# Kernel tuning notes

Measured on AMD Instinct MI355X. Metric: run time of the kernel, lower is better.

## Reference

```python
import jax, jax.numpy as jnp
import numpy as np

B, V_IN, V_OUT, F_IN, F_OUT, N_CP = 100000, 128, 128, 512, 512, 16
DIM_H = max(V_IN, V_OUT)  # hidden_vectors=None -> max(dim_vectors_in, dim_vectors_out)
EPS = 1e-8


def setup_inputs() -> dict:
    key = jax.random.key(0)
    ks = jax.random.split(key, 9)
    u = lambda k, shape, scale: jax.random.uniform(k, shape, jnp.float32, -scale, scale)
    wh_k = 1.0 / np.sqrt(V_IN).astype(np.float32)
    wu_k = 1.0 / np.sqrt(DIM_H + N_CP).astype(np.float32)
    f_in = DIM_H + N_CP + F_IN  # 656
    kf = 1.0 / np.sqrt(f_in).astype(np.float32)
    kg = 1.0 / np.sqrt(F_OUT).astype(np.float32)
    return {
        "feats": jax.random.normal(ks[0], (B, F_IN), jnp.float32),
        "vectors": jax.random.normal(ks[1], (B, V_IN, 3), jnp.float32),
        "Wh": u(ks[2], (V_IN, DIM_H), wh_k),
        "Wcp": u(ks[3], (V_IN, 2 * N_CP), wh_k),
        "Wu": u(ks[4], (DIM_H + N_CP, V_OUT), wu_k),
        "Wf": u(ks[5], (f_in, F_OUT), kf),      # torch Linear weight, stored (in,out)
        "bf": u(ks[6], (F_OUT,), kf),
        "Wg": u(ks[7], (F_OUT, V_OUT), kg),
        "bg": u(ks[8], (V_OUT,), kg),
    }


def reference(feats, vectors, Wh, Wcp, Wu, Wf, bf, Wg, bg):
    # vectors: [b, v_in, 3]; mix vector channels (matmul acts per xyz component c)
    Vh = jnp.einsum('bvc,vh->bhc', vectors, Wh)            # [b, dim_h, 3]
    # cross-product features
    Vcp = jnp.einsum('bvc,vp->bpc', vectors, Wcp)          # [b, 2*n_cp, 3]
    cp = jnp.cross(Vcp[:, :N_CP], Vcp[:, N_CP:])           # [b, n_cp, 3]
    Vh = jnp.concatenate([Vh, cp], axis=1)                 # [b, dim_h+n_cp, 3]
    Vu = jnp.einsum('bkc,ko->boc', Vh, Wu)                 # [b, v_out, 3]
    # clamped L2 norm over xyz
    sh = jnp.sqrt(jnp.maximum(jnp.sum(Vh * Vh, axis=-1), EPS))  # [b, dim_h+n_cp]
    s = jnp.concatenate([feats, sh], axis=1)               # [b, dim_h+n_cp+f_in]
    feats_out = jax.nn.silu(s @ Wf + bf)                   # [b, f_out]
    gating = feats_out @ Wg + bg                           # [b, v_out]
    vectors_out = jax.nn.sigmoid(gating)[..., None] * Vu   # [b, v_out, 3]
    return feats_out, vectors_out
```

## Files before the change

### kernel.cpp

```cpp
#include <hip/hip_runtime.h>

#define BATCH 100000
#define M3 300000
#define VECBASE 51200000
#define KP 704

typedef float fl4  __attribute__((ext_vector_type(4)));
typedef float f32x4 __attribute__((ext_vector_type(4)));
typedef short s16x4 __attribute__((ext_vector_type(4)));
typedef short s16x8 __attribute__((ext_vector_type(8)));

__device__ __forceinline__ short f2bf(float f) {
  unsigned int u = __float_as_uint(f);
  u += 0x7fffu + ((u >> 16) & 1u);
  return (short)(u >> 16);
}
__device__ __forceinline__ float bf2f(short s) {
  return __uint_as_float(((unsigned int)(unsigned short)s) << 16);
}
__device__ __forceinline__ s16x8 pack8(fl4 a, fl4 b) {
  s16x8 o;
  o[0] = f2bf(a[0]); o[1] = f2bf(a[1]); o[2] = f2bf(a[2]); o[3] = f2bf(a[3]);
  o[4] = f2bf(b[0]); o[5] = f2bf(b[1]); o[6] = f2bf(b[2]); o[7] = f2bf(b[3]);
  return o;
}
__device__ __forceinline__ void glds16(const void* g, void* l) {
  __builtin_amdgcn_global_load_lds((const __attribute__((address_space(1))) void*)g,
                                   (__attribute__((address_space(3))) void*)l, 16, 0, 0);
}

__global__ __launch_bounds__(256) void prep_w(
    const float* __restrict__ feats, const float* __restrict__ Wh,
    const float* __restrict__ Wcp, const float* __restrict__ Wu,
    const float* __restrict__ Wf, const float* __restrict__ Wg,
    short* __restrict__ Ab, short* __restrict__ WB1, short* __restrict__ WuTp,
    short* __restrict__ WfT, short* __restrict__ WgT) {
  const int tid = blockIdx.x * 256 + threadIdx.x;
  const int stride = gridDim.x * 256;
  for (int i = tid; i < 6400000; i += stride) {
    int b = i >> 6, kk = (i & 63) * 8;
    fl4 v0 = *reinterpret_cast<const fl4*>(&feats[(size_t)b * 512 + kk]);
    fl4 v1 = *reinterpret_cast<const fl4*>(&feats[(size_t)b * 512 + kk + 4]);
    *(s16x8*)&Ab[(size_t)b * KP + kk] = pack8(v0, v1);
  }
  for (int gid = tid; gid < 466944; gid += stride) {
    if (gid < 20480) {
      int n = gid >> 7, k = gid & 127;
      WB1[gid] = f2bf(n < 128 ? Wh[k * 128 + n] : Wcp[k * 32 + (n - 128)]);
    } else if (gid < 40960) {
      int i = gid - 20480;
      int o = i / 160, k = i - o * 160;
      WuTp[i] = k < 144 ? f2bf(Wu[k * 128 + o]) : (short)0;
    } else if (gid < 401408) {
      int i = gid - 40960;
      int n = i / KP, k = i - n * KP;
      WfT[i] = k < 656 ? f2bf(Wf[k * 512 + n]) : (short)0;
    } else {
      int i = gid - 401408;
      int n = i >> 9, k = i & 511;
      WgT[i] = f2bf(Wg[k * 128 + n]);
    }
  }
}

__global__ __launch_bounds__(256) void geo_fused(
    const float* __restrict__ vecs, const short* __restrict__ WB1,
    const short* __restrict__ WuTp, short* __restrict__ Ab,
    short* __restrict__ Vub) {
  __shared__ __align__(16) short U[192 * 168];
  const int t = threadIdx.x;
  const int b0 = blockIdx.x * 64;
  const int row0 = blockIdx.x * 192;

#pragma unroll
  for (int it = 0; it < 8; ++it) {
    int fi = (it * 256 + t) * 12;
    int bl = fi / 384;
    int rem = fi - bl * 384;
    int v0 = rem / 3;
    int b = b0 + bl;
    fl4 x = (fl4){0.f, 0.f, 0.f, 0.f}, y = x, z = x;
    if (b < BATCH) {
      const float* p = &vecs[(size_t)b * 384 + rem];
      x = *(const fl4*)p; y = *(const fl4*)(p + 4); z = *(const fl4*)(p + 8);
    }
    float vc[3][4] = {{x[0], x[3], y[2], z[1]},
                      {x[1], y[0], y[3], z[2]},
                      {x[2], y[1], z[0], z[3]}};
#pragma unroll
    for (int c = 0; c < 3; ++c) {
      int row = bl * 3 + c;
      s16x4 q;
#pragma unroll
      for (int e = 0; e < 4; ++e) q[e] = f2bf(vc[c][e]);
      int off = (row << 8) + (v0 << 1);
      *(s16x4*)((char*)U + (off ^ ((row & 7) << 4))) = q;
    }
  }
  __syncthreads();

  const int lane = t & 63, wv = t >> 6;
  const int wr = wv >> 1, wc = wv & 1;
  const int lr = lane & 15, lk = lane >> 4;

  {
    f32x4 acc[6][5];
#pragma unroll
    for (int i = 0; i < 6; ++i)
#pragma unroll
      for (int j = 0; j < 5; ++j) acc[i][j] = (f32x4){0.f, 0.f, 0.f, 0.f};
#pragma unroll
    for (int kk = 0; kk < 4; ++kk) {
      s16x8 af[6], bq[5];
#pragma unroll
      for (int mi = 0; mi < 6; ++mi) {
        int row = wr * 96 + mi * 16 + lr;
        int off = (row << 8) + (kk << 6) + (lk << 4);
        af[mi] = *(const s16x8*)((const char*)U + (off ^ ((row & 7) << 4)));
      }
#pragma unroll
      for (int ni = 0; ni < 5; ++ni)
        bq[ni] = *reinterpret_cast<const s16x8*>(
            &WB1[(wc * 80 + ni * 16 + lr) * 128 + (kk << 5) + (lk << 3)]);
      __builtin_amdgcn_s_setprio(1);
#pragma unroll
      for (int mi = 0; mi < 6; ++mi)
#pragma unroll
        for (int ni = 0; ni < 5; ++ni)
          acc[mi][ni] = __builtin_amdgcn_mfma_f32_16x16x32_bf16(af[mi], bq[ni], acc[mi][ni], 0, 0, 0);
      __builtin_amdgcn_s_setprio(0);
    }
    __syncthreads();
#pragma unroll
    for (int mi = 0; mi < 6; ++mi)
#pragma unroll
      for (int ni = 0; ni < 5; ++ni) {
        int col = wc * 80 + ni * 16 + lr;
#pragma unroll
        for (int r = 0; r < 4; ++r) {
          int row = wr * 96 + mi * 16 + lk * 4 + r;
          U[row * 168 + col] = f2bf(acc[mi][ni][r]);
        }
      }
  }
  __syncthreads();

  {
    int bl = t >> 2, pj = t & 3;
    int gb = b0 + bl;
    float shcp[4];
#pragma unroll
    for (int q = 0; q < 4; ++q) {
      int p = pj * 4 + q;
      float ax = bf2f(U[(bl * 3 + 0) * 168 + 128 + p]);
      float ay = bf2f(U[(bl * 3 + 1) * 168 + 128 + p]);
      float az = bf2f(U[(bl * 3 + 2) * 168 + 128 + p]);
      float bx = bf2f(U[(bl * 3 + 0) * 168 + 144 + p]);
      float by = bf2f(U[(bl * 3 + 1) * 168 + 144 + p]);
      float bz = bf2f(U[(bl * 3 + 2) * 168 + 144 + p]);
      float cx = ay * bz - az * by;
      float cy = az * bx - ax * bz;
      float cz = ax * by - ay * bx;
      U[(bl * 3 + 0) * 168 + 128 + p] = f2bf(cx);
      U[(bl * 3 + 1) * 168 + 128 + p] = f2bf(cy);
      U[(bl * 3 + 2) * 168 + 128 + p] = f2bf(cz);
      U[(bl * 3 + 0) * 168 + 144 + p] = 0;
      U[(bl * 3 + 1) * 168 + 144 + p] = 0;
      U[(bl * 3 + 2) * 168 + 144 + p] = 0;
      shcp[q] = sqrtf(fmaxf(cx * cx + cy * cy + cz * cz, 1e-8f));
    }
    if (gb < BATCH) {
#pragma unroll
      for (int q = 0; q < 4; ++q)
        Ab[(size_t)gb * KP + 512 + 128 + pj * 4 + q] = f2bf(shcp[q]);
#pragma unroll
      for (int z = 0; z < 12; ++z)
        Ab[(size_t)gb * KP + 512 + 144 + pj * 12 + z] = 0;
    }
  }
  {
    int bl = t >> 2, kq = t & 3;
    int gb = b0 + bl;
    if (gb < BATCH) {
#pragma unroll
      for (int j = 0; j < 4; ++j) {
        int k = kq * 32 + j * 8;
        s16x8 r0 = *(const s16x8*)&U[(bl * 3 + 0) * 168 + k];
        s16x8 r1 = *(const s16x8*)&U[(bl * 3 + 1) * 168 + k];
        s16x8 r2 = *(const s16x8*)&U[(bl * 3 + 2) * 168 + k];
        s16x8 o;
#pragma unroll
        for (int e = 0; e < 8; ++e) {
          float x = bf2f(r0[e]), y = bf2f(r1[e]), z = bf2f(r2[e]);
          o[e] = f2bf(sqrtf(fmaxf(x * x + y * y + z * z, 1e-8f)));
        }
        *(s16x8*)&Ab[(size_t)gb * KP + 512 + k] = o;
      }
    }
  }
  __syncthreads();

  {
    f32x4 acc2[6][4];
#pragma unroll
    for (int i = 0; i < 6; ++i)
#pragma unroll
      for (int j = 0; j < 4; ++j) acc2[i][j] = (f32x4){0.f, 0.f, 0.f, 0.f};
#pragma unroll
    for (int kk = 0; kk < 5; ++kk) {
      s16x8 af[6], bq[4];
#pragma unroll
      for (int mi = 0; mi < 6; ++mi) {
        int row = wr * 96 + mi * 16 + lr;
        af[mi] = *(const s16x8*)&U[row * 168 + (kk << 5) + (lk << 3)];
      }
#pragma unroll
      for (int ni = 0; ni < 4; ++ni)
        bq[ni] = *reinterpret_cast<const s16x8*>(
            &WuTp[(wc * 64 + ni * 16 + lr) * 160 + (kk << 5) + (lk << 3)]);
      __builtin_amdgcn_s_setprio(1);
#pragma unroll
      for (int mi = 0; mi < 6; ++mi)
#pragma unroll
        for (int ni = 0; ni < 4; ++ni)
          acc2[mi][ni] = __builtin_amdgcn_mfma_f32_16x16x32_bf16(af[mi], bq[ni], acc2[mi][ni], 0, 0, 0);
      __builtin_amdgcn_s_setprio(0);
    }
#pragma unroll
    for (int mi = 0; mi < 6; ++mi)
#pragma unroll
      for (int ni = 0; ni < 4; ++ni) {
        int col = wc * 64 + ni * 16 + lr;
#pragma unroll
        for (int r = 0; r < 4; ++r) {
          int row = row0 + wr * 96 + mi * 16 + lk * 4 + r;
          if (row < M3) Vub[(size_t)row * 128 + col] = f2bf(acc2[mi][ni][r]);
        }
      }
  }
}

__global__ __launch_bounds__(512, 4) void gemm_feats(
    const short* __restrict__ Ab, const short* __restrict__ WfT,
    const float* __restrict__ bfv, float* __restrict__ out,
    short* __restrict__ fob) {
  const int bid = blockIdx.x;
  const int xcd = bid & 7, bi = bid >> 3;
  const int swz = (xcd < 4 ? xcd * 196 : 784 + (xcd - 4) * 195) + bi;
  const int mt = swz >> 1, nt = swz & 1;
  const int row0 = mt << 7, n0 = nt << 8;
  const int t = threadIdx.x;
  const int lane = t & 63, wv = t >> 6;
  const int wr = wv >> 2, wc = wv & 3;
  const int lr = lane & 15, lk = lane >> 4;

  __shared__ __align__(16) short S[(128 + 256) * 64];
  short* As = S;
  short* Bs = S + 128 * 64;

  const short* srcA[2]; int adof[2];
#pragma unroll
  for (int j = 0; j < 2; ++j) {
    int cid = j * 512 + t;
    int row = cid >> 3, ch = cid & 7;
    srcA[j] = &Ab[(size_t)min(row0 + row, BATCH - 1) * KP + (ch ^ (row & 7)) * 8];
    adof[j] = cid * 8;
  }
  const short* srcB[4]; int bdof[4];
#pragma unroll
  for (int j = 0; j < 4; ++j) {
    int cid = j * 512 + t;
    int row = cid >> 3, ch = cid & 7;
    srcB[j] = &WfT[(size_t)(n0 + row) * KP + (ch ^ (row & 7)) * 8];
    bdof[j] = cid * 8;
  }

  f32x4 acc[4][4];
#pragma unroll
  for (int i = 0; i < 4; ++i)
#pragma unroll
    for (int j = 0; j < 4; ++j) acc[i][j] = (f32x4){0.f, 0.f, 0.f, 0.f};

  for (int ks = 0; ks < 11; ++ks) {
    const int k0 = ks << 6;
    __syncthreads();
    glds16(srcA[0] + k0, &As[adof[0]]);
    glds16(srcA[1] + k0, &As[adof[1]]);
#pragma unroll
    for (int j = 0; j < 4; ++j) glds16(srcB[j] + k0, &Bs[bdof[j]]);
    __syncthreads();
#pragma unroll
    for (int kk = 0; kk < 2; ++kk) {
      s16x8 af[4], bq[4];
#pragma unroll
      for (int mi = 0; mi < 4; ++mi) {
        int rw = wr * 64 + mi * 16 + lr;
        af[mi] = *(const s16x8*)&As[rw * 64 + (((kk << 2) + lk) ^ (rw & 7)) * 8];
      }
#pragma unroll
      for (int ni = 0; ni < 4; ++ni) {
        int rn = wc * 64 + ni * 16 + lr;
        bq[ni] = *(const s16x8*)&Bs[rn * 64 + (((kk << 2) + lk) ^ (rn & 7)) * 8];
      }
      __builtin_amdgcn_s_setprio(1);
#pragma unroll
      for (int mi = 0; mi < 4; ++mi)
#pragma unroll
        for (int ni = 0; ni < 4; ++ni)
          acc[mi][ni] = __builtin_amdgcn_mfma_f32_16x16x32_bf16(af[mi], bq[ni], acc[mi][ni], 0, 0, 0);
      __builtin_amdgcn_s_setprio(0);
    }
  }

  float* Ls = (float*)S;
#pragma unroll
  for (int g = 0; g < 8; ++g) {
    __syncthreads();
    if (wr == (g >> 2)) {
      int mi = g & 3;
#pragma unroll
      for (int ni = 0; ni < 4; ++ni) {
        int colL = wc * 64 + ni * 16 + lr;
        float bb = bfv[n0 + colL];
#pragma unroll
        for (int rr = 0; rr < 4; ++rr) {
          float x = acc[mi][ni][rr] + bb;
          Ls[(lk * 4 + rr) * 256 + colL] = x / (1.f + __expf(-x));
        }
      }
    }
    __syncthreads();
    {
      int rowL = t >> 5, seg = t & 31;
      int grow = row0 + g * 16 + rowL;
      if (grow < BATCH) {
        const float* p = &Ls[rowL * 256 + seg * 8];
        fl4 a = *(const fl4*)p, b = *(const fl4*)(p + 4);
        float* po = &out[(size_t)grow * 512 + n0 + seg * 8];
        *(fl4*)po = a; *(fl4*)(po + 4) = b;
        *(s16x8*)&fob[(size_t)grow * 512 + n0 + seg * 8] = pack8(a, b);
      }
    }
  }
}

__global__ __launch_bounds__(512, 4) void gemm_gate(
    const short* __restrict__ fob, const short* __restrict__ WgT,
    const float* __restrict__ bg, const short* __restrict__ Vub,
    float* __restrict__ out) {
  const int bid = blockIdx.x;
  const int xcd = bid & 7, bi = bid >> 3;
  const int swz = (xcd < 7 ? xcd * 49 : 343 + (xcd - 7) * 48) + bi;
  const int row0 = swz << 8;
  const int t = threadIdx.x;
  const int lane = t & 63, wv = t >> 6;
  const int wr = wv >> 1, wc = wv & 1;
  const int lr = lane & 15, lk = lane >> 4;

  __shared__ __align__(16) short S[(256 + 128) * 64];
  short* As = S;
  short* Bs = S + 256 * 64;

  const short* srcA[4]; int adof[4];
#pragma unroll
  for (int j = 0; j < 4; ++j) {
    int cid = j * 512 + t;
    int row = cid >> 3, ch = cid & 7;
    srcA[j] = &fob[(size_t)min(row0 + row, BATCH - 1) * 512 + (ch ^ (row & 7)) * 8];
    adof[j] = cid * 8;
  }
  const short* srcB[2]; int bdof[2];
#pragma unroll
  for (int j = 0; j < 2; ++j) {
    int cid = j * 512 + t;
    int row = cid >> 3, ch = cid & 7;
    srcB[j] = &WgT[(size_t)row * 512 + (ch ^ (row & 7)) * 8];
    bdof[j] = cid * 8;
  }

  f32x4 acc[4][4];
#pragma unroll
  for (int i = 0; i < 4; ++i)
#pragma unroll
    for (int j = 0; j < 4; ++j) acc[i][j] = (f32x4){0.f, 0.f, 0.f, 0.f};

  for (int ks = 0; ks < 8; ++ks) {
    const int k0 = ks << 6;
    __syncthreads();
#pragma unroll
    for (int j = 0; j < 4; ++j) glds16(srcA[j] + k0, &As[adof[j]]);
    glds16(srcB[0] + k0, &Bs[bdof[0]]);
    glds16(srcB[1] + k0, &Bs[bdof[1]]);
    __syncthreads();
#pragma unroll
    for (int kk = 0; kk < 2; ++kk) {
      s16x8 af[4], bq[4];
#pragma unroll
      for (int mi = 0; mi < 4; ++mi) {
        int rw = wr * 64 + mi * 16 + lr;
        af[mi] = *(const s16x8*)&As[rw * 64 + (((kk << 2) + lk) ^ (rw & 7)) * 8];
      }
#pragma unroll
      for (int ni = 0; ni < 4; ++ni) {
        int rn = wc * 64 + ni * 16 + lr;
        bq[ni] = *(const s16x8*)&Bs[rn * 64 + (((kk << 2) + lk) ^ (rn & 7)) * 8];
      }
      __builtin_amdgcn_s_setprio(1);
#pragma unroll
      for (int mi = 0; mi < 4; ++mi)
#pragma unroll
        for (int ni = 0; ni < 4; ++ni)
          acc[mi][ni] = __builtin_amdgcn_mfma_f32_16x16x32_bf16(af[mi], bq[ni], acc[mi][ni], 0, 0, 0);
      __builtin_amdgcn_s_setprio(0);
    }
  }

#pragma unroll
  for (int ni = 0; ni < 4; ++ni) {
    int col = wc * 64 + ni * 16 + lr;
    float bb = bg[col];
#pragma unroll
    for (int mi = 0; mi < 4; ++mi) {
      int rbase = row0 + wr * 64 + mi * 16 + lk * 4;
#pragma unroll
      for (int rr = 0; rr < 4; ++rr) {
        int gr = rbase + rr;
        if (gr < BATCH) {
          float x = acc[mi][ni][rr] + bb;
          float gate = 1.f / (1.f + __expf(-x));
          size_t vb = (size_t)(3 * gr) * 128 + col;
          float* po = &out[VECBASE + ((size_t)gr * 128 + col) * 3];
          po[0] = gate * bf2f(Vub[vb]);
          po[1] = gate * bf2f(Vub[vb + 128]);
          po[2] = gate * bf2f(Vub[vb + 256]);
        }
      }
    }
  }
}

extern "C" void kernel_launch(void* const* d_in, const int* in_sizes, int n_in,
                              void* d_out, int out_size, void* d_ws, size_t ws_size,
                              hipStream_t stream) {
  const float* feats = (const float*)d_in[0];
  const float* vecs  = (const float*)d_in[1];
  const float* Wh    = (const float*)d_in[2];
  const float* Wcp   = (const float*)d_in[3];
  const float* Wu    = (const float*)d_in[4];
  const float* Wf    = (const float*)d_in[5];
  const float* bfv   = (const float*)d_in[6];
  const float* Wg    = (const float*)d_in[7];
  const float* bg    = (const float*)d_in[8];
  float* out = (float*)d_out;

  char* ws = (char*)d_ws;
  short* Ab   = (short*)ws;
  short* Vub  = (short*)(ws + 140800000);
  short* fob  = (short*)(ws + 217600000);
  short* WfT  = (short*)(ws + 320000000);
  short* WgT  = (short*)(ws + 320720896);
  short* WB1  = (short*)(ws + 320851968);
  short* WuTp = (short*)(ws + 320892928);

  hipLaunchKernelGGL(prep_w,     dim3(2048), dim3(256), 0, stream,
                     feats, Wh, Wcp, Wu, Wf, Wg, Ab, WB1, WuTp, WfT, WgT);
  hipLaunchKernelGGL(geo_fused,  dim3(1563), dim3(256), 0, stream,
                     vecs, WB1, WuTp, Ab, Vub);
  hipLaunchKernelGGL(gemm_feats, dim3(1564), dim3(512), 0, stream,
                     Ab, WfT, bfv, out, fob);
  hipLaunchKernelGGL(gemm_gate,  dim3(391),  dim3(512), 0, stream,
                     fob, WgT, bg, Vub, out);
}
```

Before: 432.9 us.

## Double-buffer feature GEMM K-loop and halve geo kernel batch tile

The feature GEMM now uses two LDS buffers with 32-wide K slices, issuing async global-to-LDS loads two stages ahead and synchronising with raw s_waitcnt/s_barrier, so load latency overlaps MFMA work instead of a sync-load-sync per step. The geo kernel processes 32 batch rows per block instead of 64, doubling the grid and shrinking LDS and accumulator usage to raise occupancy. Bounds checks are dropped because 100000 divides evenly by 32. The hand-written vmcnt counts must match the number of outstanding loads, and the K-slice swizzle changed to fit the narrower tiles.

```diff
diff --git a/kernel.cpp b/kernel.cpp
--- a/kernel.cpp
+++ b/kernel.cpp
@@ -28,6 +28,8 @@
   __builtin_amdgcn_global_load_lds((const __attribute__((address_space(1))) void*)g,
                                    (__attribute__((address_space(3))) void*)l, 16, 0, 0);
 }
+#define WAITBAR(N) asm volatile("s_waitcnt vmcnt(" #N ")\ns_barrier" ::: "memory")
+#define RAWBAR()   asm volatile("s_barrier" ::: "memory")
 
 __global__ __launch_bounds__(256) void prep_w(
     const float* __restrict__ feats, const float* __restrict__ Wh,
@@ -67,23 +69,19 @@
     const float* __restrict__ vecs, const short* __restrict__ WB1,
     const short* __restrict__ WuTp, short* __restrict__ Ab,
     short* __restrict__ Vub) {
-  __shared__ __align__(16) short U[192 * 168];
+  __shared__ __align__(16) short U[96 * 168];
   const int t = threadIdx.x;
-  const int b0 = blockIdx.x * 64;
-  const int row0 = blockIdx.x * 192;
-
-#pragma unroll
-  for (int it = 0; it < 8; ++it) {
+  const int b0 = blockIdx.x * 32;
+  const int row0 = blockIdx.x * 96;
+
+#pragma unroll
+  for (int it = 0; it < 4; ++it) {
     int fi = (it * 256 + t) * 12;
     int bl = fi / 384;
     int rem = fi - bl * 384;
     int v0 = rem / 3;
-    int b = b0 + bl;
-    fl4 x = (fl4){0.f, 0.f, 0.f, 0.f}, y = x, z = x;
-    if (b < BATCH) {
-      const float* p = &vecs[(size_t)b * 384 + rem];
-      x = *(const fl4*)p; y = *(const fl4*)(p + 4); z = *(const fl4*)(p + 8);
-    }
+    const float* p = &vecs[(size_t)(b0 + bl) * 384 + rem];
+    fl4 x = *(const fl4*)p, y = *(const fl4*)(p + 4), z = *(const fl4*)(p + 8);
     float vc[3][4] = {{x[0], x[3], y[2], z[1]},
                       {x[1], y[0], y[3], z[2]},
                       {x[2], y[1], z[0], z[3]}};
@@ -104,17 +102,17 @@
   const int lr = lane & 15, lk = lane >> 4;
 
   {
-    f32x4 acc[6][5];
-#pragma unroll
-    for (int i = 0; i < 6; ++i)
+    f32x4 acc[3][5];
+#pragma unroll
+    for (int i = 0; i < 3; ++i)
 #pragma unroll
       for (int j = 0; j < 5; ++j) acc[i][j] = (f32x4){0.f, 0.f, 0.f, 0.f};
 #pragma unroll
     for (int kk = 0; kk < 4; ++kk) {
-      s16x8 af[6], bq[5];
-#pragma unroll
-      for (int mi = 0; mi < 6; ++mi) {
-        int row = wr * 96 + mi * 16 + lr;
+      s16x8 af[3], bq[5];
+#pragma unroll
+      for (int mi = 0; mi < 3; ++mi) {
+        int row = wr * 48 + mi * 16 + lr;
         int off = (row << 8) + (kk << 6) + (lk << 4);
         af[mi] = *(const s16x8*)((const char*)U + (off ^ ((row & 7) << 4)));
       }
@@ -124,7 +122,7 @@
             &WB1[(wc * 80 + ni * 16 + lr) * 128 + (kk << 5) + (lk << 3)]);
       __builtin_amdgcn_s_setprio(1);
 #pragma unroll
-      for (int mi = 0; mi < 6; ++mi)
+      for (int mi = 0; mi < 3; ++mi)
 #pragma unroll
         for (int ni = 0; ni < 5; ++ni)
           acc[mi][ni] = __builtin_amdgcn_mfma_f32_16x16x32_bf16(af[mi], bq[ni], acc[mi][ni], 0, 0, 0);
@@ -132,13 +130,13 @@
     }
     __syncthreads();
 #pragma unroll
-    for (int mi = 0; mi < 6; ++mi)
+    for (int mi = 0; mi < 3; ++mi)
 #pragma unroll
       for (int ni = 0; ni < 5; ++ni) {
         int col = wc * 80 + ni * 16 + lr;
 #pragma unroll
         for (int r = 0; r < 4; ++r) {
-          int row = wr * 96 + mi * 16 + lk * 4 + r;
+          int row = wr * 48 + mi * 16 + lk * 4 + r;
           U[row * 168 + col] = f2bf(acc[mi][ni][r]);
         }
       }
@@ -146,12 +144,12 @@
   __syncthreads();
 
   {
-    int bl = t >> 2, pj = t & 3;
+    int bl = t >> 3, pj = t & 7;
     int gb = b0 + bl;
-    float shcp[4];
-#pragma unroll
-    for (int q = 0; q < 4; ++q) {
-      int p = pj * 4 + q;
+    float shcp[2];
+#pragma unroll
+    for (int q = 0; q < 2; ++q) {
+      int p = pj * 2 + q;
       float ax = bf2f(U[(bl * 3 + 0) * 168 + 128 + p]);
       float ay = bf2f(U[(bl * 3 + 1) * 168 + 128 + p]);
       float az = bf2f(U[(bl * 3 + 2) * 168 + 128 + p]);
@@ -169,49 +167,44 @@
       U[(bl * 3 + 2) * 168 + 144 + p] = 0;
       shcp[q] = sqrtf(fmaxf(cx * cx + cy * cy + cz * cz, 1e-8f));
     }
-    if (gb < BATCH) {
-#pragma unroll
-      for (int q = 0; q < 4; ++q)
-        Ab[(size_t)gb * KP + 512 + 128 + pj * 4 + q] = f2bf(shcp[q]);
-#pragma unroll
-      for (int z = 0; z < 12; ++z)
-        Ab[(size_t)gb * KP + 512 + 144 + pj * 12 + z] = 0;
-    }
+    Ab[(size_t)gb * KP + 640 + pj * 2]     = f2bf(shcp[0]);
+    Ab[(size_t)gb * KP + 640 + pj * 2 + 1] = f2bf(shcp[1]);
+#pragma unroll
+    for (int z = 0; z < 6; ++z)
+      Ab[(size_t)gb * KP + 656 + pj * 6 + z] = 0;
   }
   {
-    int bl = t >> 2, kq = t & 3;
+    int bl = t >> 3, kq = t & 7;
     int gb = b0 + bl;
-    if (gb < BATCH) {
-#pragma unroll
-      for (int j = 0; j < 4; ++j) {
-        int k = kq * 32 + j * 8;
-        s16x8 r0 = *(const s16x8*)&U[(bl * 3 + 0) * 168 + k];
-        s16x8 r1 = *(const s16x8*)&U[(bl * 3 + 1) * 168 + k];
-        s16x8 r2 = *(const s16x8*)&U[(bl * 3 + 2) * 168 + k];
-        s16x8 o;
-#pragma unroll
-        for (int e = 0; e < 8; ++e) {
-          float x = bf2f(r0[e]), y = bf2f(r1[e]), z = bf2f(r2[e]);
-          o[e] = f2bf(sqrtf(fmaxf(x * x + y * y + z * z, 1e-8f)));
-        }
-        *(s16x8*)&Ab[(size_t)gb * KP + 512 + k] = o;
-      }
+#pragma unroll
+    for (int j = 0; j < 2; ++j) {
+      int k = kq * 16 + j * 8;
+      s16x8 r0 = *(const s16x8*)&U[(bl * 3 + 0) * 168 + k];
+      s16x8 r1 = *(const s16x8*)&U[(bl * 3 + 1) * 168 + k];
+      s16x8 r2 = *(const s16x8*)&U[(bl * 3 + 2) * 168 + k];
+      s16x8 o;
+#pragma unroll
+      for (int e = 0; e < 8; ++e) {
+        float x = bf2f(r0[e]), y = bf2f(r1[e]), z = bf2f(r2[e]);
+        o[e] = f2bf(sqrtf(fmaxf(x * x + y * y + z * z, 1e-8f)));
+      }
+      *(s16x8*)&Ab[(size_t)gb * KP + 512 + k] = o;
     }
   }
   __syncthreads();
 
   {
-    f32x4 acc2[6][4];
-#pragma unroll
-    for (int i = 0; i < 6; ++i)
+    f32x4 acc2[3][4];
+#pragma unroll
+    for (int i = 0; i < 3; ++i)
 #pragma unroll
       for (int j = 0; j < 4; ++j) acc2[i][j] = (f32x4){0.f, 0.f, 0.f, 0.f};
 #pragma unroll
     for (int kk = 0; kk < 5; ++kk) {
-      s16x8 af[6], bq[4];
-#pragma unroll
-      for (int mi = 0; mi < 6; ++mi) {
-        int row = wr * 96 + mi * 16 + lr;
+      s16x8 af[3], bq[4];
+#pragma unroll
+      for (int mi = 0; mi < 3; ++mi) {
+        int row = wr * 48 + mi * 16 + lr;
         af[mi] = *(const s16x8*)&U[row * 168 + (kk << 5) + (lk << 3)];
       }
 #pragma unroll
@@ -220,21 +213,21 @@
             &WuTp[(wc * 64 + ni * 16 + lr) * 160 + (kk << 5) + (lk << 3)]);
       __builtin_amdgcn_s_setprio(1);
 #pragma unroll
-      for (int mi = 0; mi < 6; ++mi)
+      for (int mi = 0; mi < 3; ++mi)
 #pragma unroll
         for (int ni = 0; ni < 4; ++ni)
           acc2[mi][ni] = __builtin_amdgcn_mfma_f32_16x16x32_bf16(af[mi], bq[ni], acc2[mi][ni], 0, 0, 0);
       __builtin_amdgcn_s_setprio(0);
     }
 #pragma unroll
-    for (int mi = 0; mi < 6; ++mi)
+    for (int mi = 0; mi < 3; ++mi)
 #pragma unroll
       for (int ni = 0; ni < 4; ++ni) {
         int col = wc * 64 + ni * 16 + lr;
 #pragma unroll
         for (int r = 0; r < 4; ++r) {
-          int row = row0 + wr * 96 + mi * 16 + lk * 4 + r;
-          if (row < M3) Vub[(size_t)row * 128 + col] = f2bf(acc2[mi][ni][r]);
+          int row = row0 + wr * 48 + mi * 16 + lk * 4 + r;
+          Vub[(size_t)row * 128 + col] = f2bf(acc2[mi][ni][r]);
         }
       }
   }
@@ -254,24 +247,19 @@
   const int wr = wv >> 2, wc = wv & 3;
   const int lr = lane & 15, lk = lane >> 4;
 
-  __shared__ __align__(16) short S[(128 + 256) * 64];
-  short* As = S;
-  short* Bs = S + 128 * 64;
-
-  const short* srcA[2]; int adof[2];
+  __shared__ __align__(16) short As[2][128 * 32];
+  __shared__ __align__(16) short Bs[2][256 * 32];
+
+  const int arow = t >> 2, ach = t & 3;
+  const short* srcA = &Ab[(size_t)min(row0 + arow, BATCH - 1) * KP +
+                          ((ach ^ ((arow >> 1) & 3))) * 8];
+  const int adof = t * 8;
+  const short* srcB[2]; int bdof[2];
 #pragma unroll
   for (int j = 0; j < 2; ++j) {
     int cid = j * 512 + t;
-    int row = cid >> 3, ch = cid & 7;
-    srcA[j] = &Ab[(size_t)min(row0 + row, BATCH - 1) * KP + (ch ^ (row & 7)) * 8];
-    adof[j] = cid * 8;
-  }
-  const short* srcB[4]; int bdof[4];
-#pragma unroll
-  for (int j = 0; j < 4; ++j) {
-    int cid = j * 512 + t;
-    int row = cid >> 3, ch = cid & 7;
-    srcB[j] = &WfT[(size_t)(n0 + row) * KP + (ch ^ (row & 7)) * 8];
+    int brow = cid >> 2, bch = cid & 3;
+    srcB[j] = &WfT[(size_t)(n0 + brow) * KP + ((bch ^ ((brow >> 1) & 3))) * 8];
     bdof[j] = cid * 8;
   }
 
@@ -281,38 +269,44 @@
 #pragma unroll
     for (int j = 0; j < 4; ++j) acc[i][j] = (f32x4){0.f, 0.f, 0.f, 0.f};
 
-  for (int ks = 0; ks < 11; ++ks) {
-    const int k0 = ks << 6;
-    __syncthreads();
-    glds16(srcA[0] + k0, &As[adof[0]]);
-    glds16(srcA[1] + k0, &As[adof[1]]);
-#pragma unroll
-    for (int j = 0; j < 4; ++j) glds16(srcB[j] + k0, &Bs[bdof[j]]);
-    __syncthreads();
-#pragma unroll
-    for (int kk = 0; kk < 2; ++kk) {
-      s16x8 af[4], bq[4];
-#pragma unroll
-      for (int mi = 0; mi < 4; ++mi) {
-        int rw = wr * 64 + mi * 16 + lr;
-        af[mi] = *(const s16x8*)&As[rw * 64 + (((kk << 2) + lk) ^ (rw & 7)) * 8];
-      }
-#pragma unroll
-      for (int ni = 0; ni < 4; ++ni) {
-        int rn = wc * 64 + ni * 16 + lr;
-        bq[ni] = *(const s16x8*)&Bs[rn * 64 + (((kk << 2) + lk) ^ (rn & 7)) * 8];
-      }
-      __builtin_amdgcn_s_setprio(1);
-#pragma unroll
-      for (int mi = 0; mi < 4; ++mi)
-#pragma unroll
-        for (int ni = 0; ni < 4; ++ni)
-          acc[mi][ni] = __builtin_amdgcn_mfma_f32_16x16x32_bf16(af[mi], bq[ni], acc[mi][ni], 0, 0, 0);
-      __builtin_amdgcn_s_setprio(0);
-    }
-  }
-
-  float* Ls = (float*)S;
+  auto STAGE = [&](int buf, int ks) {
+    const int k0 = ks << 5;
+    glds16(srcA + k0, &As[buf][adof]);
+    glds16(srcB[0] + k0, &Bs[buf][bdof[0]]);
+    glds16(srcB[1] + k0, &Bs[buf][bdof[1]]);
+  };
+  auto COMPUTE = [&](int buf) {
+    s16x8 af[4], bq[4];
+#pragma unroll
+    for (int mi = 0; mi < 4; ++mi) {
+      int rw = wr * 64 + mi * 16 + lr;
+      af[mi] = *(const s16x8*)&As[buf][rw * 32 + (lk ^ ((rw >> 1) & 3)) * 8];
+    }
+#pragma unroll
+    for (int ni = 0; ni < 4; ++ni) {
+      int rn = wc * 64 + ni * 16 + lr;
+      bq[ni] = *(const s16x8*)&Bs[buf][rn * 32 + (lk ^ ((rn >> 1) & 3)) * 8];
+    }
+    __builtin_amdgcn_s_setprio(1);
+#pragma unroll
+    for (int mi = 0; mi < 4; ++mi)
+#pragma unroll
+      for (int ni = 0; ni < 4; ++ni)
+        acc[mi][ni] = __builtin_amdgcn_mfma_f32_16x16x32_bf16(af[mi], bq[ni], acc[mi][ni], 0, 0, 0);
+    __builtin_amdgcn_s_setprio(0);
+  };
+
+  STAGE(0, 0);
+  STAGE(1, 1);
+  for (int ks = 0; ks < 22; ++ks) {
+    if (ks < 21) WAITBAR(3);
+    else         WAITBAR(0);
+    COMPUTE(ks & 1);
+    RAWBAR();
+    if (ks + 2 < 22) STAGE(ks & 1, ks + 2);
+  }
+
+  float* Ls = (float*)&As[0][0];
 #pragma unroll
   for (int g = 0; g < 8; ++g) {
     __syncthreads();
@@ -464,7 +458,7 @@
 
   hipLaunchKernelGGL(prep_w,     dim3(2048), dim3(256), 0, stream,
                      feats, Wh, Wcp, Wu, Wf, Wg, Ab, WB1, WuTp, WfT, WgT);
-  hipLaunchKernelGGL(geo_fused,  dim3(1563), dim3(256), 0, stream,
+  hipLaunchKernelGGL(geo_fused,  dim3(3125), dim3(256), 0, stream,
                      vecs, WB1, WuTp, Ab, Vub);
   hipLaunchKernelGGL(gemm_feats, dim3(1564), dim3(512), 0, stream,
                      Ab, WfT, bfv, out, fob);
```

Measured after the change: 435.7 us. No clear change (+0.7%).
